# Kernel tuning notes

Measured on AMD Instinct MI355X. Metric: run time of the kernel, lower is better.

## Reference

```python
import jax, jax.numpy as jnp
import numpy as np

HEAD_DIM = 64
N_HEADS = 64
N_KV = 8
Q_MULT = N_HEADS // N_KV  # 8
HIDDEN = 2880
SEQ = 1024
BATCH = 2
SLIDING_WINDOW = 128  # layer_idx=0 -> window active
ROPE_THETA = 150000.0
SCALING = 32.0
NTK_ALPHA = 1.0
NTK_BETA = 32.0
INIT_CTX = 4096
EPS = 1e-5


def _rope_caches(seq_len):
    # YaRN rotary caches (static numpy precompute, as in the source module)
    steps = np.arange(0, HEAD_DIM, 2, dtype=np.float32)
    freq = np.power(np.float32(ROPE_THETA), steps / np.float32(HEAD_DIM))
    concentration = np.float32(0.1) * np.log(np.float32(SCALING)) + 1.0
    d_half = np.float32(HEAD_DIM / 2.0)
    log_base = np.log(np.float32(ROPE_THETA))
    low = d_half * np.log(np.float32(INIT_CTX) / (np.float32(NTK_BETA) * np.float32(2.0 * np.pi))) / log_base
    high = d_half * np.log(np.float32(INIT_CTX) / (np.float32(NTK_ALPHA) * np.float32(2.0 * np.pi))) / log_base
    ramp = (np.arange(HEAD_DIM // 2, dtype=np.float32) - low) / (high - low)
    mask = 1.0 - np.clip(ramp, 0.0, 1.0)
    inv_freq = (1.0 / (np.float32(SCALING) * freq)) * (1.0 - mask) + (1.0 / freq) * mask
    pos = np.arange(seq_len, dtype=np.float32)
    freqs = np.einsum('i,j->ij', pos, inv_freq.astype(np.float32))
    cos = (np.cos(freqs) * concentration).astype(np.float32)
    sin = (np.sin(freqs) * concentration).astype(np.float32)
    return jnp.asarray(cos), jnp.asarray(sin)


def _apply_rotary(t, cos, sin):
    # t: (B, S, ..., head_dim); cos/sin: (S, head_dim//2). Rotate-half style.
    shape = (1, t.shape[1]) + (1,) * (t.ndim - 3) + (cos.shape[-1],)
    c = cos.reshape(shape)
    s = sin.reshape(shape)
    first, second = jnp.split(t, 2, axis=-1)
    return jnp.concatenate([first * c - second * s, second * c + first * s], axis=-1)


def setup_inputs() -> dict:
    key = jax.random.key(0)
    ks = jax.random.split(key, 6)
    qkv_dim = (N_HEADS + 2 * N_KV) * HEAD_DIM  # 5120
    return {
        'x': jax.random.normal(ks[0], (BATCH, SEQ, HIDDEN), dtype=jnp.float32),
        'norm_w': jnp.ones((HIDDEN,), dtype=jnp.float32),
        'qkv_w': jax.random.normal(ks[1], (qkv_dim, HIDDEN), dtype=jnp.float32) * 0.02,
        'qkv_b': jax.random.normal(ks[2], (qkv_dim,), dtype=jnp.float32) * 0.02,
        'out_w': jax.random.normal(ks[3], (HIDDEN, N_HEADS * HEAD_DIM), dtype=jnp.float32) * 0.02,
        'out_b': jax.random.normal(ks[4], (HIDDEN,), dtype=jnp.float32) * 0.02,
        'sinks': jax.random.normal(ks[5], (N_HEADS,), dtype=jnp.float32),
    }


def reference(x, norm_w, qkv_w, qkv_b, out_w, out_b, sinks):
    B, S, _ = x.shape
    # RMSNorm (fp32 accumulation)
    xf = x.astype(jnp.float32)
    rms = jnp.mean(xf * xf, axis=-1, keepdims=True)
    t = (xf * jax.lax.rsqrt(rms + EPS) * norm_w).astype(x.dtype)
    # QKV projection (fp32 accumulation)
    qkv = jnp.matmul(t.astype(jnp.float32), qkv_w.T) + qkv_b
    q_dim = N_HEADS * HEAD_DIM
    kv_dim = N_KV * HEAD_DIM
    q = qkv[..., :q_dim].reshape(B, S, N_KV, Q_MULT, HEAD_DIM)
    k = qkv[..., q_dim:q_dim + kv_dim].reshape(B, S, N_KV, HEAD_DIM)
    v = qkv[..., q_dim + kv_dim:].reshape(B, S, N_KV, HEAD_DIM)
    # YaRN rotary embedding
    cos, sin = _rope_caches(S)
    q = _apply_rotary(q, cos, sin)
    k = _apply_rotary(k, cos, sin)
    # causal + sliding-window mask
    neg_inf = jnp.float32(-jnp.inf)
    mask = jnp.triu(jnp.full((S, S), neg_inf, dtype=jnp.float32), k=1)
    mask = mask + jnp.tril(jnp.full((S, S), neg_inf, dtype=jnp.float32), k=-SLIDING_WINDOW)
    sm_scale = jnp.float32(1.0 / np.sqrt(HEAD_DIM))
    # GQA attention with sink logits
    logits = jnp.einsum('bqhmd,bkhd->bhmqk', q, k) * sm_scale + mask[None, None, None]
    sink = jnp.broadcast_to(sinks.reshape(1, N_KV, Q_MULT, 1, 1), (B, N_KV, Q_MULT, S, 1))
    logits = jnp.concatenate([logits, sink], axis=-1)
    w = jax.nn.softmax(logits, axis=-1)[..., :-1]  # drop sink column
    attn = jnp.einsum('bhmqk,bkhd->bqhmd', w, v).reshape(B, S, N_HEADS * HEAD_DIM)
    # output projection (fp32 accumulation) + residual
    out = jnp.matmul(attn, out_w.T) + out_b
    return x + out
```

## Files before the change

kernel.cpp:

```cpp
#include <hip/hip_runtime.h>

typedef unsigned short ushort_t;
typedef __attribute__((ext_vector_type(8))) short short8;
typedef __attribute__((ext_vector_type(8))) __bf16 bf16x8;
typedef __attribute__((ext_vector_type(4))) float float4v;
typedef __attribute__((ext_vector_type(4))) unsigned int uint4v;

__device__ __forceinline__ float bf2f(ushort_t u) {
    unsigned int v = ((unsigned int)u) << 16;
    return __builtin_bit_cast(float, v);
}
__device__ __forceinline__ ushort_t f2bf(float f) {
    unsigned int u = __builtin_bit_cast(unsigned int, f);
    unsigned int lsb = (u >> 16) & 1u;
    u += 0x7fffu + lsb;
    return (ushort_t)(u >> 16);
}
__device__ __forceinline__ uint4v pack8(const ushort_t* r) {
    uint4v u;
#pragma unroll
    for (int i = 0; i < 4; ++i)
        u[i] = (unsigned int)r[2 * i] | ((unsigned int)r[2 * i + 1] << 16);
    return u;
}
__device__ __forceinline__ void unpack8(uint4v u, float* f) {
#pragma unroll
    for (int i = 0; i < 4; ++i) {
        unsigned int x = u[i];
        f[2 * i] = __builtin_bit_cast(float, x << 16);
        f[2 * i + 1] = __builtin_bit_cast(float, x & 0xffff0000u);
    }
}
__device__ __forceinline__ uint4v ld8f32_bf(const float* p) {
    float4v a = *(const float4v*)p;
    float4v b = *(const float4v*)(p + 4);
    ushort_t r[8];
#pragma unroll
    for (int j = 0; j < 4; ++j) { r[j] = f2bf(a[j]); r[4 + j] = f2bf(b[j]); }
    return pack8(r);
}

#if __has_builtin(__builtin_amdgcn_global_load_lds)
#define HAVE_GLDS 1
__device__ __forceinline__ void glds16(const ushort_t* gp, ushort_t* lp) {
    __builtin_amdgcn_global_load_lds((const __attribute__((address_space(1))) void*)gp,
                                     (__attribute__((address_space(3))) void*)lp, 16, 0, 0);
}
#else
#define HAVE_GLDS 0
#endif

template <typename V>
__device__ __forceinline__ auto mfma_sel(V a, V b, float4v c, int)
    -> decltype(__builtin_amdgcn_mfma_f32_16x16x32_bf16(a, b, c, 0, 0, 0)) {
    return __builtin_amdgcn_mfma_f32_16x16x32_bf16(a, b, c, 0, 0, 0);
}
template <typename V>
__device__ __forceinline__ float4v mfma_sel(V a, V b, float4v c, long) {
    return __builtin_amdgcn_mfma_f32_16x16x32_bf16(__builtin_bit_cast(bf16x8, a),
                                                   __builtin_bit_cast(bf16x8, b), c, 0, 0, 0);
}
__device__ __forceinline__ float4v mfma_bf16(short8 a, short8 b, float4v c) {
    return mfma_sel(a, b, c, 0);
}

__device__ __forceinline__ float wave_sum(float v) {
#pragma unroll
    for (int o = 32; o; o >>= 1) v += __shfl_xor(v, o);
    return v;
}

#define HIDDEN 2880
#define NTOK 2048
#define QKV_DIM 5120
#define ATTN_DIM 4096
#define SM_SCALE 0.125f

__global__ __launch_bounds__(256) void f32_to_bf16_dual_kernel(const float* __restrict__ a,
                                                               ushort_t* __restrict__ ao, int na8,
                                                               const float* __restrict__ b,
                                                               ushort_t* __restrict__ bo, int nb8) {
    int idx = blockIdx.x * 256 + threadIdx.x;
    if (idx < na8) {
        *(uint4v*)(ao + (size_t)idx * 8) = ld8f32_bf(a + (size_t)idx * 8);
    } else {
        int j = idx - na8;
        if (j < nb8) *(uint4v*)(bo + (size_t)j * 8) = ld8f32_bf(b + (size_t)j * 8);
    }
}

__global__ __launch_bounds__(256) void rmsnorm_kernel(const float* __restrict__ x,
                                                      const float* __restrict__ wgt,
                                                      ushort_t* __restrict__ out) {
    const int tok = blockIdx.x, tid = threadIdx.x;
    const float* xr = x + (size_t)tok * HIDDEN;
    float v[16];
    float ss = 0.f;
#pragma unroll
    for (int i = 0; i < 2; ++i) {
        int c = tid + i * 256;
        if (c < 360) {
            float4v a = *(const float4v*)(xr + c * 8);
            float4v b = *(const float4v*)(xr + c * 8 + 4);
#pragma unroll
            for (int j = 0; j < 4; ++j) { v[i * 8 + j] = a[j]; v[i * 8 + 4 + j] = b[j]; }
#pragma unroll
            for (int j = 0; j < 8; ++j) ss += v[i * 8 + j] * v[i * 8 + j];
        }
    }
    ss = wave_sum(ss);
    __shared__ float red[4];
    if ((tid & 63) == 0) red[tid >> 6] = ss;
    __syncthreads();
    float scale = rsqrtf((red[0] + red[1] + red[2] + red[3]) * (1.f / 2880.f) + 1e-5f);
#pragma unroll
    for (int i = 0; i < 2; ++i) {
        int c = tid + i * 256;
        if (c < 360) {
            float4v wa = *(const float4v*)(wgt + c * 8);
            float4v wb = *(const float4v*)(wgt + c * 8 + 4);
            ushort_t r[8];
#pragma unroll
            for (int j = 0; j < 4; ++j) {
                r[j] = f2bf(v[i * 8 + j] * scale * wa[j]);
                r[4 + j] = f2bf(v[i * 8 + 4 + j] * scale * wb[j]);
            }
            *(uint4v*)(out + (size_t)tok * HIDDEN + c * 8) = pack8(r);
        }
    }
}

__global__ __launch_bounds__(256) void rope_apply_kernel(ushort_t* __restrict__ qkv) {
    int idx = blockIdx.x * 256 + threadIdx.x;
    int tok = idx / 288;
    int rem = idx - tok * 288;
    int h = rem >> 2, dg = rem & 3;
    int s = tok & 1023;
    size_t base = (size_t)tok * QKV_DIM + (h < 64 ? h * 64 : 4096 + (h - 64) * 64) + dg * 8;
    uint4v u1 = *(const uint4v*)(qkv + base);
    uint4v u2 = *(const uint4v*)(qkv + base + 32);
    float f1[8], f2[8];
    unpack8(u1, f1);
    unpack8(u2, f2);
    const float step = (float)(11.918390573078392 / 32.0);
    const float conc = (float)(1.3465735902799727);
    const float low = (float)(8.092890725542669);
    const float invden = (float)(1.0 / 9.305804387286162);
    ushort_t r1[8], r2[8];
#pragma unroll
    for (int jj = 0; jj < 8; ++jj) {
        int j = dg * 8 + jj;
        float invf = __expf(-(float)j * step);
        float ramp = ((float)j - low) * invden;
        float mask = 1.f - fminf(fmaxf(ramp, 0.f), 1.f);
        float inv_freq = invf * ((1.f - mask) * 0.03125f + mask);
        float ang = (float)s * inv_freq;
        float c = __cosf(ang) * conc;
        float sn = __sinf(ang) * conc;
        r1[jj] = f2bf(f1[jj] * c - f2[jj] * sn);
        r2[jj] = f2bf(f2[jj] * c + f1[jj] * sn);
    }
    *(uint4v*)(qkv + base) = pack8(r1);
    *(uint4v*)(qkv + base + 32) = pack8(r2);
}

template <int BN, bool RESID, bool OUTF32, bool BF16B>
__global__ __launch_bounds__(256) void gemm_kernel(const ushort_t* __restrict__ A,
                                                   const void* __restrict__ B,
                                                   const float* __restrict__ bias,
                                                   const float* __restrict__ resid,
                                                   void* __restrict__ Cout, int M, int N, int K) {
    constexpr int BM = 128, BK = 64;
    constexpr bool GL = BF16B && (HAVE_GLDS != 0);
    constexpr int LDT = GL ? 64 : 72;
    constexpr int NBUF = GL ? 2 : 1;
    static_assert(BN == 160 || BN == 128 || BN == 96 || BN == 64, "");
    __shared__ __align__(16) ushort_t As[NBUF][BM * LDT];
    __shared__ __align__(16) ushort_t Bs[NBUF][BN * LDT];

    const int nbx = gridDim.x;
    int wg = blockIdx.y * nbx + blockIdx.x;
    {
        const int nwg = nbx * gridDim.y;
        const int cpx = nwg >> 3;
        wg = (wg & 7) * cpx + (wg >> 3);
    }
    const int m0 = (wg / nbx) * BM;
    const int n0 = (wg % nbx) * BN;
    const int tid = threadIdx.x;
    const int w = tid >> 6, lane = tid & 63;
    const int quad = lane >> 4, l16 = lane & 15;

    constexpr int WN = BN / 2;
    constexpr int NI = WN / 16;
    const int wm = (w >> 1) * 64;
    const int wn = (w & 1) * WN;

    float4v acc[4][NI];
#pragma unroll
    for (int i = 0; i < 4; ++i)
#pragma unroll
        for (int j = 0; j < NI; ++j) acc[i][j] = (float4v){0.f, 0.f, 0.f, 0.f};

    const int nk = K / BK;

#if HAVE_GLDS
    if constexpr (GL) {
        constexpr int NAI = BM / 32;
        constexpr int NBI = BN / 32;
        const ushort_t* Bp = (const ushort_t*)B;
        const ushort_t* agp[NAI];
        const ushort_t* bgp[NBI];
        ushort_t* alp[2][NAI];
        ushort_t* blp[2][NBI];
#pragma unroll
        for (int i = 0; i < NAI; ++i) {
            int sb = (w * NAI + i) * 64;
            int s = sb + lane, r = s >> 3, p = s & 7, c = p ^ (r & 7);
            agp[i] = A + (size_t)(m0 + r) * K + c * 8;
            alp[0][i] = &As[0][sb * 8];
            alp[1][i] = &As[1][sb * 8];
        }
#pragma unroll
        for (int i = 0; i < NBI; ++i) {
            int sb = (w * NBI + i) * 64;
            int s = sb + lane, r = s >> 3, p = s & 7, c = p ^ (r & 7);
            bgp[i] = Bp + (size_t)(n0 + r) * K + c * 8;
            blp[0][i] = &Bs[0][sb * 8];
            blp[1][i] = &Bs[1][sb * 8];
        }
#pragma unroll
        for (int i = 0; i < NAI; ++i) glds16(agp[i], alp[0][i]);
#pragma unroll
        for (int i = 0; i < NBI; ++i) glds16(bgp[i], blp[0][i]);
        __syncthreads();

        for (int kt = 0; kt < nk; ++kt) {
            const int cur = kt & 1;
            if (kt + 1 < nk) {
                const int k0 = (kt + 1) * BK;
#pragma unroll
                for (int i = 0; i < NAI; ++i) glds16(agp[i] + k0, alp[cur ^ 1][i]);
#pragma unroll
                for (int i = 0; i < NBI; ++i) glds16(bgp[i] + k0, blp[cur ^ 1][i]);
            }
            const ushort_t* Asb = As[cur];
            const ushort_t* Bsb = Bs[cur];
#pragma unroll
            for (int ks = 0; ks < 2; ++ks) {
                short8 af[4], bfr[NI];
#pragma unroll
                for (int mi = 0; mi < 4; ++mi) {
                    int row = wm + mi * 16 + l16;
                    af[mi] = *(const short8*)(Asb + row * LDT + ((ks * 4 + quad) ^ (row & 7)) * 8);
                }
#pragma unroll
                for (int ni = 0; ni < NI; ++ni) {
                    int row = wn + ni * 16 + l16;
                    bfr[ni] = *(const short8*)(Bsb + row * LDT + ((ks * 4 + quad) ^ (row & 7)) * 8);
                }
#pragma unroll
                for (int mi = 0; mi < 4; ++mi)
#pragma unroll
                    for (int ni = 0; ni < NI; ++ni)
                        acc[mi][ni] = mfma_bf16(af[mi], bfr[ni], acc[mi][ni]);
            }
            __syncthreads();
        }
    } else
#endif
    {
        constexpr int ACH = BM * BK / 8 / 256;
        constexpr int BCH = BN * BK / 8 / 256;
        uint4v areg[ACH], breg[BCH];
#pragma unroll
        for (int i = 0; i < ACH; ++i) {
            int c = tid + i * 256, r = c >> 3, col = c & 7;
            areg[i] = *(const uint4v*)(A + (size_t)(m0 + r) * K + col * 8);
        }
#pragma unroll
        for (int i = 0; i < BCH; ++i) {
            int c = tid + i * 256, r = c >> 3, col = c & 7;
            if constexpr (BF16B)
                breg[i] = *(const uint4v*)((const ushort_t*)B + (size_t)(n0 + r) * K + col * 8);
            else
                breg[i] = ld8f32_bf((const float*)B + (size_t)(n0 + r) * K + col * 8);
        }
        for (int kt = 0; kt < nk; ++kt) {
            __syncthreads();
#pragma unroll
            for (int i = 0; i < ACH; ++i) {
                int c = tid + i * 256, r = c >> 3, col = c & 7;
                *(uint4v*)(&As[0][r * LDT + col * 8]) = areg[i];
            }
#pragma unroll
            for (int i = 0; i < BCH; ++i) {
                int c = tid + i * 256, r = c >> 3, col = c & 7;
                *(uint4v*)(&Bs[0][r * LDT + col * 8]) = breg[i];
            }
            __syncthreads();
            if (kt + 1 < nk) {
                const int k0 = (kt + 1) * BK;
#pragma unroll
                for (int i = 0; i < ACH; ++i) {
                    int c = tid + i * 256, r = c >> 3, col = c & 7;
                    areg[i] = *(const uint4v*)(A + (size_t)(m0 + r) * K + k0 + col * 8);
                }
#pragma unroll
                for (int i = 0; i < BCH; ++i) {
                    int c = tid + i * 256, r = c >> 3, col = c & 7;
                    if constexpr (BF16B)
                        breg[i] = *(const uint4v*)((const ushort_t*)B + (size_t)(n0 + r) * K + k0 + col * 8);
                    else
                        breg[i] = ld8f32_bf((const float*)B + (size_t)(n0 + r) * K + k0 + col * 8);
                }
            }
#pragma unroll
            for (int ks = 0; ks < 2; ++ks) {
                short8 af[4], bfr[NI];
#pragma unroll
                for (int mi = 0; mi < 4; ++mi)
                    af[mi] = *(const short8*)(&As[0][(wm + mi * 16 + l16) * LDT + ks * 32 + quad * 8]);
#pragma unroll
                for (int ni = 0; ni < NI; ++ni)
                    bfr[ni] = *(const short8*)(&Bs[0][(wn + ni * 16 + l16) * LDT + ks * 32 + quad * 8]);
#pragma unroll
                for (int mi = 0; mi < 4; ++mi)
#pragma unroll
                    for (int ni = 0; ni < NI; ++ni)
                        acc[mi][ni] = mfma_bf16(af[mi], bfr[ni], acc[mi][ni]);
            }
        }
    }

#pragma unroll
    for (int ni = 0; ni < NI; ++ni) {
        int gc = n0 + wn + ni * 16 + l16;
        float bv = bias[gc];
#pragma unroll
        for (int mi = 0; mi < 4; ++mi) {
#pragma unroll
            for (int r = 0; r < 4; ++r) {
                int gr = m0 + wm + mi * 16 + quad * 4 + r;
                float vv = acc[mi][ni][r] + bv;
                if constexpr (RESID) vv += resid[(size_t)gr * N + gc];
                if constexpr (OUTF32) ((float*)Cout)[(size_t)gr * N + gc] = vv;
                else ((ushort_t*)Cout)[(size_t)gr * N + gc] = f2bf(vv);
            }
        }
    }
}

__global__ __launch_bounds__(256, 2) void attn_mfma_kernel(const ushort_t* __restrict__ qkv,
                                                           const float* __restrict__ sinks,
                                                           ushort_t* __restrict__ attnbuf) {
    constexpr int LDK = 72, LDV = 200, LDP = 200;
    __shared__ __align__(16) ushort_t Ks[192 * LDK];
    __shared__ __align__(16) ushort_t Vt[64 * LDV];
    __shared__ __align__(16) ushort_t Pb[4][16 * LDP];

    const int qc = blockIdx.x, kvh = blockIdx.y >> 1, half = blockIdx.y & 1, b = blockIdx.z;
    const int tid = threadIdx.x;
    const int w = tid >> 6, lane = tid & 63;
    const int quad = lane >> 4, l16 = lane & 15;
    const int w0 = qc * 64 - 127;

    for (int c = tid; c < 192 * 8; c += 256) {
        int row = c >> 3, col8 = c & 7;
        int pos = w0 + row;
        pos = pos < 0 ? 0 : (pos > 1023 ? 1023 : pos);
        size_t gk = ((size_t)(b * 1024 + pos)) * QKV_DIM + 4096 + kvh * 64 + col8 * 8;
        *(uint4v*)(Ks + row * LDK + col8 * 8) = *(const uint4v*)(qkv + gk);
        uint4v vv = *(const uint4v*)(qkv + gk + 512);
        ushort_t vs[8];
#pragma unroll
        for (int i = 0; i < 4; ++i) {
            vs[2 * i] = (ushort_t)(vv[i] & 0xffffu);
            vs[2 * i + 1] = (ushort_t)(vv[i] >> 16);
        }
#pragma unroll
        for (int j = 0; j < 8; ++j) Vt[(col8 * 8 + j) * LDV + row] = vs[j];
    }
    __syncthreads();

    ushort_t* Pw = Pb[w];
    const int h = kvh * 8 + half * 4 + w;
    const float sink_f = sinks[h];

    for (int p = 0; p < 2; ++p) {
        short8 Vf[5][4];
#pragma unroll
        for (int j = 0; j < 5; ++j)
#pragma unroll
            for (int nv = 0; nv < 4; ++nv)
                Vf[j][nv] = *(const short8*)(Vt + (nv * 16 + l16) * LDV + (p + j) * 32 + quad * 8);

#pragma unroll
        for (int qq = 0; qq < 2; ++qq) {
            const int qtile = 2 * p + qq;
            const int tokb = b * 1024 + qc * 64 + qtile * 16;

            short8 qf[2];
            {
                const ushort_t* qp = qkv + ((size_t)(tokb + l16)) * QKV_DIM + h * 64 + quad * 8;
                qf[0] = *(const short8*)qp;
                qf[1] = *(const short8*)(qp + 32);
            }

            float4v acc[9];
#pragma unroll
            for (int j = 0; j < 9; ++j) acc[j] = (float4v){0.f, 0.f, 0.f, 0.f};
            __builtin_amdgcn_s_setprio(1);
#pragma unroll
            for (int j = 0; j < 9; ++j) {
                const int nt = qtile + j;
#pragma unroll
                for (int ks = 0; ks < 2; ++ks) {
                    short8 kf = *(const short8*)(Ks + (nt * 16 + l16) * LDK + ks * 32 + quad * 8);
                    acc[j] = mfma_bf16(qf[ks], kf, acc[j]);
                }
            }
            __builtin_amdgcn_s_setprio(0);

            const int ntz = qq ? (qtile - 1) : (qtile + 9);

            float linv[4];
#pragma unroll
            for (int r = 0; r < 4; ++r) {
                const int ql = qtile * 16 + quad * 4 + r;
                float e[9];
                float mx = -1e30f;
#pragma unroll
                for (int j = 0; j < 9; ++j) {
                    int row_k = (qtile + j) * 16 + l16;
                    bool valid = (row_k >= ql) && (row_k <= ql + 127) && (w0 + row_k >= 0);
                    float s = valid ? acc[j][r] * SM_SCALE : -1e30f;
                    e[j] = s;
                    mx = fmaxf(mx, s);
                }
#pragma unroll
                for (int o = 1; o < 16; o <<= 1) mx = fmaxf(mx, __shfl_xor(mx, o));
                float M = fmaxf(mx, sink_f);
                float ls = 0.f;
#pragma unroll
                for (int j = 0; j < 9; ++j) {
                    float ev = (e[j] > -1e29f) ? __expf(e[j] - M) : 0.f;
                    e[j] = ev;
                    ls += ev;
                }
#pragma unroll
                for (int o = 1; o < 16; o <<= 1) ls += __shfl_xor(ls, o);
                linv[r] = 1.f / (ls + __expf(sink_f - M));
#pragma unroll
                for (int j = 0; j < 9; ++j)
                    Pw[(quad * 4 + r) * LDP + (qtile + j) * 16 + l16] = f2bf(e[j]);
                Pw[(quad * 4 + r) * LDP + ntz * 16 + l16] = 0;
            }

            float4v accO[4];
#pragma unroll
            for (int nv = 0; nv < 4; ++nv) accO[nv] = (float4v){0.f, 0.f, 0.f, 0.f};
            __builtin_amdgcn_s_setprio(1);
#pragma unroll
            for (int j = 0; j < 5; ++j) {
                short8 pf = *(const short8*)(Pw + l16 * LDP + (p + j) * 32 + quad * 8);
#pragma unroll
                for (int nv = 0; nv < 4; ++nv) accO[nv] = mfma_bf16(pf, Vf[j][nv], accO[nv]);
            }
            __builtin_amdgcn_s_setprio(0);

#pragma unroll
            for (int r = 0; r < 4; ++r) {
                size_t ob = ((size_t)(tokb + quad * 4 + r)) * ATTN_DIM + h * 64 + l16;
#pragma unroll
                for (int nv = 0; nv < 4; ++nv)
                    attnbuf[ob + nv * 16] = f2bf(accO[nv][r] * linv[r]);
            }
        }
    }
}

extern "C" void kernel_launch(void* const* d_in, const int* in_sizes, int n_in,
                              void* d_out, int out_size, void* d_ws, size_t ws_size,
                              hipStream_t stream) {
    const float* x = (const float*)d_in[0];
    const float* norm_w = (const float*)d_in[1];
    const float* qkv_w = (const float*)d_in[2];
    const float* qkv_b = (const float*)d_in[3];
    const float* out_w = (const float*)d_in[4];
    const float* out_b = (const float*)d_in[5];
    const float* sinks = (const float*)d_in[6];
    float* outp = (float*)d_out;
    char* ws = (char*)d_ws;

    if (ws_size >= 86000000ull) {
        ushort_t* qkvbuf = (ushort_t*)ws;
        ushort_t* qkv_w_bf = (ushort_t*)(ws + 20971520);
        ushort_t* attnbuf = (ushort_t*)(ws + 20971520);
        ushort_t* out_w_bf = (ushort_t*)(ws + 50462720);
        ushort_t* Tbuf = (ushort_t*)d_out;

        f32_to_bf16_dual_kernel<<<12960, 256, 0, stream>>>(qkv_w, qkv_w_bf, 1843200,
                                                           out_w, out_w_bf, 1474560);
        rmsnorm_kernel<<<NTOK, 256, 0, stream>>>(x, norm_w, Tbuf);
        gemm_kernel<160, false, false, true><<<dim3(32, 16), 256, 0, stream>>>(
            Tbuf, qkv_w_bf, qkv_b, nullptr, qkvbuf, NTOK, QKV_DIM, HIDDEN);
        rope_apply_kernel<<<2304, 256, 0, stream>>>(qkvbuf);
        attn_mfma_kernel<<<dim3(16, 16, 2), 256, 0, stream>>>(qkvbuf, sinks, attnbuf);
        gemm_kernel<96, true, true, true><<<dim3(30, 16), 256, 0, stream>>>(
            attnbuf, out_w_bf, out_b, x, outp, NTOK, HIDDEN, ATTN_DIM);
    } else {
        ushort_t* qkvbuf = (ushort_t*)ws;
        ushort_t* attnbuf = (ushort_t*)(ws + 20971520);
        ushort_t* Tbuf = (ushort_t*)d_out;

        rmsnorm_kernel<<<NTOK, 256, 0, stream>>>(x, norm_w, Tbuf);
        gemm_kernel<128, false, false, false><<<dim3(40, 16), 256, 0, stream>>>(
            Tbuf, qkv_w, qkv_b, nullptr, qkvbuf, NTOK, QKV_DIM, HIDDEN);
        rope_apply_kernel<<<2304, 256, 0, stream>>>(qkvbuf);
        attn_mfma_kernel<<<dim3(16, 16, 2), 256, 0, stream>>>(qkvbuf, sinks, attnbuf);
        gemm_kernel<96, true, true, false><<<dim3(30, 16), 256, 0, stream>>>(
            attnbuf, out_w, out_b, x, outp, NTOK, HIDDEN, ATTN_DIM);
    }
}
```

Before: 315.0 us.

## Fuse RoPE into attention loads and merge rmsnorm with weight conversion

Removes the standalone RoPE kernel and applies the rotary embedding on the fly when K tiles are staged into shared memory and when Q fragments are loaded in the attention kernel. RMSNorm and the fp32-to-bf16 weight conversion are merged into a single prep launch. This saves a full read/write pass over the QKV buffer and two kernel launches. In exchange, K rows are rotated redundantly across overlapping windows and by both head halves, and the attention kernel gains trig work and register pressure.

```diff
diff --git a/kernel.cpp b/kernel.cpp
--- a/kernel.cpp
+++ b/kernel.cpp
@@ -76,16 +76,71 @@
 #define ATTN_DIM 4096
 #define SM_SCALE 0.125f
 
-__global__ __launch_bounds__(256) void f32_to_bf16_dual_kernel(const float* __restrict__ a,
-                                                               ushort_t* __restrict__ ao, int na8,
-                                                               const float* __restrict__ b,
-                                                               ushort_t* __restrict__ bo, int nb8) {
-    int idx = blockIdx.x * 256 + threadIdx.x;
-    if (idx < na8) {
-        *(uint4v*)(ao + (size_t)idx * 8) = ld8f32_bf(a + (size_t)idx * 8);
+#define ROPE_STEP 0.37244970540869975f
+#define ROPE_CONC 1.3465735902799727f
+#define ROPE_LOW 8.092890725542669f
+#define ROPE_INVDEN 0.10745959154836568f
+
+__device__ __forceinline__ float rope_invfreq(int j) {
+    float invf = __expf(-(float)j * ROPE_STEP);
+    float ramp = ((float)j - ROPE_LOW) * ROPE_INVDEN;
+    float mask = 1.f - fminf(fmaxf(ramp, 0.f), 1.f);
+    return invf * ((1.f - mask) * 0.03125f + mask);
+}
+
+__global__ __launch_bounds__(256) void prep_kernel(const float* __restrict__ x,
+                                                   const float* __restrict__ wgt,
+                                                   ushort_t* __restrict__ tout,
+                                                   const float* __restrict__ a,
+                                                   ushort_t* __restrict__ ao, int na8,
+                                                   const float* __restrict__ b,
+                                                   ushort_t* __restrict__ bo, int nb8) {
+    const int tid = threadIdx.x;
+    __shared__ float red[4];
+    if (blockIdx.x < NTOK) {
+        const int tok = blockIdx.x;
+        const float* xr = x + (size_t)tok * HIDDEN;
+        float v[16];
+        float ss = 0.f;
+#pragma unroll
+        for (int i = 0; i < 2; ++i) {
+            int c = tid + i * 256;
+            if (c < 360) {
+                float4v va = *(const float4v*)(xr + c * 8);
+                float4v vb = *(const float4v*)(xr + c * 8 + 4);
+#pragma unroll
+                for (int j = 0; j < 4; ++j) { v[i * 8 + j] = va[j]; v[i * 8 + 4 + j] = vb[j]; }
+#pragma unroll
+                for (int j = 0; j < 8; ++j) ss += v[i * 8 + j] * v[i * 8 + j];
+            }
+        }
+        ss = wave_sum(ss);
+        if ((tid & 63) == 0) red[tid >> 6] = ss;
+        __syncthreads();
+        float scale = rsqrtf((red[0] + red[1] + red[2] + red[3]) * (1.f / 2880.f) + 1e-5f);
+#pragma unroll
+        for (int i = 0; i < 2; ++i) {
+            int c = tid + i * 256;
+            if (c < 360) {
+                float4v wa = *(const float4v*)(wgt + c * 8);
+                float4v wb = *(const float4v*)(wgt + c * 8 + 4);
+                ushort_t r[8];
+#pragma unroll
+                for (int j = 0; j < 4; ++j) {
+                    r[j] = f2bf(v[i * 8 + j] * scale * wa[j]);
+                    r[4 + j] = f2bf(v[i * 8 + 4 + j] * scale * wb[j]);
+                }
+                *(uint4v*)(tout + (size_t)tok * HIDDEN + c * 8) = pack8(r);
+            }
+        }
     } else {
-        int j = idx - na8;
-        if (j < nb8) *(uint4v*)(bo + (size_t)j * 8) = ld8f32_bf(b + (size_t)j * 8);
+        int idx = (blockIdx.x - NTOK) * 256 + tid;
+        if (idx < na8) {
+            *(uint4v*)(ao + (size_t)idx * 8) = ld8f32_bf(a + (size_t)idx * 8);
+        } else {
+            int j = idx - na8;
+            if (j < nb8) *(uint4v*)(bo + (size_t)j * 8) = ld8f32_bf(b + (size_t)j * 8);
+        }
     }
 }
 
@@ -128,40 +183,6 @@
             *(uint4v*)(out + (size_t)tok * HIDDEN + c * 8) = pack8(r);
         }
     }
-}
-
-__global__ __launch_bounds__(256) void rope_apply_kernel(ushort_t* __restrict__ qkv) {
-    int idx = blockIdx.x * 256 + threadIdx.x;
-    int tok = idx / 288;
-    int rem = idx - tok * 288;
-    int h = rem >> 2, dg = rem & 3;
-    int s = tok & 1023;
-    size_t base = (size_t)tok * QKV_DIM + (h < 64 ? h * 64 : 4096 + (h - 64) * 64) + dg * 8;
-    uint4v u1 = *(const uint4v*)(qkv + base);
-    uint4v u2 = *(const uint4v*)(qkv + base + 32);
-    float f1[8], f2[8];
-    unpack8(u1, f1);
-    unpack8(u2, f2);
-    const float step = (float)(11.918390573078392 / 32.0);
-    const float conc = (float)(1.3465735902799727);
-    const float low = (float)(8.092890725542669);
-    const float invden = (float)(1.0 / 9.305804387286162);
-    ushort_t r1[8], r2[8];
-#pragma unroll
-    for (int jj = 0; jj < 8; ++jj) {
-        int j = dg * 8 + jj;
-        float invf = __expf(-(float)j * step);
-        float ramp = ((float)j - low) * invden;
-        float mask = 1.f - fminf(fmaxf(ramp, 0.f), 1.f);
-        float inv_freq = invf * ((1.f - mask) * 0.03125f + mask);
-        float ang = (float)s * inv_freq;
-        float c = __cosf(ang) * conc;
-        float sn = __sinf(ang) * conc;
-        r1[jj] = f2bf(f1[jj] * c - f2[jj] * sn);
-        r2[jj] = f2bf(f2[jj] * c + f1[jj] * sn);
-    }
-    *(uint4v*)(qkv + base) = pack8(r1);
-    *(uint4v*)(qkv + base + 32) = pack8(r2);
 }
 
 template <int BN, bool RESID, bool OUTF32, bool BF16B>
@@ -365,13 +386,40 @@
     const int quad = lane >> 4, l16 = lane & 15;
     const int w0 = qc * 64 - 127;
 
+    {
+        float invfK[8];
+#pragma unroll
+        for (int jj = 0; jj < 8; ++jj) invfK[jj] = rope_invfreq((tid & 3) * 8 + jj);
+        for (int c = tid; c < 192 * 4; c += 256) {
+            int row = c >> 2, col4 = c & 3;
+            int pos = w0 + row;
+            pos = pos < 0 ? 0 : (pos > 1023 ? 1023 : pos);
+            size_t gk = ((size_t)(b * 1024 + pos)) * QKV_DIM + 4096 + kvh * 64 + col4 * 8;
+            uint4v u1 = *(const uint4v*)(qkv + gk);
+            uint4v u2 = *(const uint4v*)(qkv + gk + 32);
+            float f1[8], f2[8];
+            unpack8(u1, f1);
+            unpack8(u2, f2);
+            float s = (float)pos;
+            ushort_t r1[8], r2[8];
+#pragma unroll
+            for (int jj = 0; jj < 8; ++jj) {
+                float ang = s * invfK[jj];
+                float cc = __cosf(ang) * ROPE_CONC;
+                float sn = __sinf(ang) * ROPE_CONC;
+                r1[jj] = f2bf(f1[jj] * cc - f2[jj] * sn);
+                r2[jj] = f2bf(f2[jj] * cc + f1[jj] * sn);
+            }
+            *(uint4v*)(Ks + row * LDK + col4 * 8) = pack8(r1);
+            *(uint4v*)(Ks + row * LDK + (col4 + 4) * 8) = pack8(r2);
+        }
+    }
     for (int c = tid; c < 192 * 8; c += 256) {
         int row = c >> 3, col8 = c & 7;
         int pos = w0 + row;
         pos = pos < 0 ? 0 : (pos > 1023 ? 1023 : pos);
-        size_t gk = ((size_t)(b * 1024 + pos)) * QKV_DIM + 4096 + kvh * 64 + col8 * 8;
-        *(uint4v*)(Ks + row * LDK + col8 * 8) = *(const uint4v*)(qkv + gk);
-        uint4v vv = *(const uint4v*)(qkv + gk + 512);
+        size_t gv = ((size_t)(b * 1024 + pos)) * QKV_DIM + 4608 + kvh * 64 + col8 * 8;
+        uint4v vv = *(const uint4v*)(qkv + gv);
         ushort_t vs[8];
 #pragma unroll
         for (int i = 0; i < 4; ++i) {
@@ -387,6 +435,10 @@
     const int h = kvh * 8 + half * 4 + w;
     const float sink_f = sinks[h];
 
+    float invfQ[8];
+#pragma unroll
+    for (int jj = 0; jj < 8; ++jj) invfQ[jj] = rope_invfreq(quad * 8 + jj);
+
     for (int p = 0; p < 2; ++p) {
         short8 Vf[5][4];
 #pragma unroll
@@ -403,8 +455,23 @@
             short8 qf[2];
             {
                 const ushort_t* qp = qkv + ((size_t)(tokb + l16)) * QKV_DIM + h * 64 + quad * 8;
-                qf[0] = *(const short8*)qp;
-                qf[1] = *(const short8*)(qp + 32);
+                uint4v u1 = *(const uint4v*)qp;
+                uint4v u2 = *(const uint4v*)(qp + 32);
+                float f1[8], f2[8];
+                unpack8(u1, f1);
+                unpack8(u2, f2);
+                float s = (float)((tokb + l16) & 1023);
+                ushort_t r1[8], r2[8];
+#pragma unroll
+                for (int jj = 0; jj < 8; ++jj) {
+                    float ang = s * invfQ[jj];
+                    float cc = __cosf(ang) * ROPE_CONC;
+                    float sn = __sinf(ang) * ROPE_CONC;
+                    r1[jj] = f2bf(f1[jj] * cc - f2[jj] * sn);
+                    r2[jj] = f2bf(f2[jj] * cc + f1[jj] * sn);
+                }
+                qf[0] = __builtin_bit_cast(short8, pack8(r1));
+                qf[1] = __builtin_bit_cast(short8, pack8(r2));
             }
 
             float4v acc[9];
@@ -500,12 +567,10 @@
         ushort_t* out_w_bf = (ushort_t*)(ws + 50462720);
         ushort_t* Tbuf = (ushort_t*)d_out;
 
-        f32_to_bf16_dual_kernel<<<12960, 256, 0, stream>>>(qkv_w, qkv_w_bf, 1843200,
-                                                           out_w, out_w_bf, 1474560);
-        rmsnorm_kernel<<<NTOK, 256, 0, stream>>>(x, norm_w, Tbuf);
+        prep_kernel<<<NTOK + 12960, 256, 0, stream>>>(x, norm_w, Tbuf, qkv_w, qkv_w_bf,
+                                                      1843200, out_w, out_w_bf, 1474560);
         gemm_kernel<160, false, false, true><<<dim3(32, 16), 256, 0, stream>>>(
             Tbuf, qkv_w_bf, qkv_b, nullptr, qkvbuf, NTOK, QKV_DIM, HIDDEN);
-        rope_apply_kernel<<<2304, 256, 0, stream>>>(qkvbuf);
         attn_mfma_kernel<<<dim3(16, 16, 2), 256, 0, stream>>>(qkvbuf, sinks, attnbuf);
         gemm_kernel<96, true, true, true><<<dim3(30, 16), 256, 0, stream>>>(
             attnbuf, out_w_bf, out_b, x, outp, NTOK, HIDDEN, ATTN_DIM);
@@ -517,7 +582,6 @@
         rmsnorm_kernel<<<NTOK, 256, 0, stream>>>(x, norm_w, Tbuf);
         gemm_kernel<128, false, false, false><<<dim3(40, 16), 256, 0, stream>>>(
             Tbuf, qkv_w, qkv_b, nullptr, qkvbuf, NTOK, QKV_DIM, HIDDEN);
-        rope_apply_kernel<<<2304, 256, 0, stream>>>(qkvbuf);
         attn_mfma_kernel<<<dim3(16, 16, 2), 256, 0, stream>>>(qkvbuf, sinks, attnbuf);
         gemm_kernel<96, true, true, false><<<dim3(30, 16), 256, 0, stream>>>(
             attnbuf, out_w, out_b, x, outp, NTOK, HIDDEN, ATTN_DIM);
```

Result: faster. 308.7 us (-2.0%).
